# Optimization experiments

Measured on AMD Instinct MI355X. Metric: run time of the kernel, lower is better.

## Reference

```python
import jax, jax.numpy as jnp
import numpy as np

T = 0.2  # temperature (init default)
EPS = 1e-12  # torch F.normalize eps


def setup_inputs() -> dict:
    key = jax.random.key(0)
    k1, k2 = jax.random.split(key, 2)
    b, in_c, out_c = 8192, 128, 128
    anchor_features = jax.random.normal(k1, (b, in_c), dtype=jnp.float32)
    W = jax.random.normal(k2, (in_c, out_c), dtype=jnp.float32) * (1.0 / np.sqrt(in_c))
    bias = jnp.zeros((out_c,), dtype=jnp.float32)
    return {"anchor_features": anchor_features, "W": W, "bias": bias}


def reference(anchor_features, W, bias):
    # MappingLayer: linear projection + L2 normalize, then pairwise cosine sims.
    z = anchor_features @ W + bias                                  # [b, d]
    z = z / jnp.maximum(jnp.linalg.norm(z, axis=-1, keepdims=True), EPS)
    sim = (z @ z.T) / T                                             # [b, b]
    b = sim.shape[0]
    idx = jnp.arange(b)
    j0 = (idx + b // 2) % b                                         # positive pair index
    # Fused symmetric exp matrix: E[i,j] = exp(sim[i,j] + sim[j,i])
    E = jnp.exp(sim + sim.T)                                        # [b, b]
    top = E[idx, j0]                                                # exp(s_ij0 + s_j0i)
    bottom = jnp.sum(E, axis=1) - E[idx, idx]                       # sum over j != i
    loss = -jnp.sum(jnp.log(top / bottom)) / (b - 1)
    return loss
```

## Files before the change

### kernel.cpp

```cpp
#include <hip/hip_runtime.h>
#include <stdint.h>

typedef short bf16x8 __attribute__((ext_vector_type(8)));
typedef float f32x4 __attribute__((ext_vector_type(4)));

#define NROWS 8192
#define DIM   128
#define ZSCALE 3.7982824f
#define LN2F  0.6931471805599453f


__device__ __forceinline__ unsigned short f32_to_bf16_bits(float x) {
  union { float f; uint32_t u; } v; v.f = x;
  uint32_t r = v.u + 0x7FFFu + ((v.u >> 16) & 1u);
  return (unsigned short)(r >> 16);
}

__global__ __launch_bounds__(256) void k_wprep(const float* __restrict__ W,
                                               unsigned short* __restrict__ Wtf,
                                               float* __restrict__ sumexp,
                                               float* __restrict__ topacc) {
  const int idx = blockIdx.x * 256 + threadIdx.x;
  if (idx < 2048) {
    const int l = idx & 63, chunk = idx >> 6;
    const int tj = chunk >> 2, ks = chunk & 3, g = l >> 4, q = l & 15;
    const float* wp = W + (size_t)(ks * 32 + g * 8) * DIM + tj * 16 + q;
    bf16x8 o;
#pragma unroll
    for (int e = 0; e < 8; ++e) o[e] = (short)f32_to_bf16_bits(wp[(size_t)e * DIM]);
    *(bf16x8*)(Wtf + (size_t)idx * 8) = o;
  }
  if (idx < NROWS) sumexp[idx] = 0.f;
  if (idx == 0) topacc[0] = 0.f;
}

__global__ __launch_bounds__(256) void k_proj_norm(
    const float* __restrict__ anchor, const unsigned short* __restrict__ Wtf,
    const float* __restrict__ bias, unsigned short* __restrict__ zf) {
  __shared__ float part[4][16][132];
  const int t = threadIdx.x;
  const int wv = t >> 6, l = t & 63, g = l >> 4, q = l & 15;
  const int rb = blockIdx.x * 16;

  const float* ap = anchor + (size_t)(rb + q) * DIM + wv * 32 + g * 8;
  const f32x4 a0 = *(const f32x4*)ap, a1 = *(const f32x4*)(ap + 4);
  bf16x8 a;
#pragma unroll
  for (int e = 0; e < 4; ++e) {
    a[e] = (short)f32_to_bf16_bits(a0[e]);
    a[4 + e] = (short)f32_to_bf16_bits(a1[e]);
  }

  f32x4 acc[8];
#pragma unroll
  for (int tj = 0; tj < 8; ++tj) acc[tj] = (f32x4){0.f, 0.f, 0.f, 0.f};
#pragma unroll
  for (int tj = 0; tj < 8; ++tj) {
    const bf16x8 b = *(const bf16x8*)(Wtf + (size_t)((tj * 4 + wv) * 64 + l) * 8);
    acc[tj] = __builtin_amdgcn_mfma_f32_16x16x32_bf16(a, b, acc[tj], 0, 0, 0);
  }

#pragma unroll
  for (int tj = 0; tj < 8; ++tj)
#pragma unroll
    for (int r = 0; r < 4; ++r) part[wv][4 * g + r][tj * 16 + q] = acc[tj][r];
  __syncthreads();

  const int row = t >> 4, c = t & 15;
  float v[8];
#pragma unroll
  for (int e = 0; e < 8; ++e) v[e] = bias[c * 8 + e];
#pragma unroll
  for (int s = 0; s < 4; ++s) {
    const f32x4 p0 = *(const f32x4*)&part[s][row][c * 8];
    const f32x4 p1 = *(const f32x4*)&part[s][row][c * 8 + 4];
#pragma unroll
    for (int e = 0; e < 4; ++e) {
      v[e] += p0[e];
      v[4 + e] += p1[e];
    }
  }
  float ss = 0.f;
#pragma unroll
  for (int e = 0; e < 8; ++e) ss += v[e] * v[e];
#pragma unroll
  for (int m = 1; m < 16; m <<= 1) ss += __shfl_xor(ss, m, 64);
  const float inv = ZSCALE / fmaxf(sqrtf(ss), 1e-12f);

  bf16x8 o;
#pragma unroll
  for (int e = 0; e < 8; ++e) o[e] = (short)f32_to_bf16_bits(v[e] * inv);
  const int ks = c >> 2, gg = c & 3;
  *(bf16x8*)(zf + (size_t)(((blockIdx.x * 4 + ks) * 64) + gg * 16 + row) * 8) = o;
}

template <int MODE>
__device__ __forceinline__ void simloss_body(
    const unsigned short* __restrict__ zf, float* __restrict__ sumexp,
    float* __restrict__ topacc, const int r0, const int cb, const int l,
    const int g, const int q) {
  bf16x8 afr[2][4];
#pragma unroll
  for (int ti = 0; ti < 2; ++ti)
#pragma unroll
    for (int ks = 0; ks < 4; ++ks)
      afr[ti][ks] = *(const bf16x8*)(
          zf + (size_t)((((r0 >> 4) + ti) * 4 + ks) * 512 + l * 8));

  float sums[2][4] = {{0.f, 0.f, 0.f, 0.f}, {0.f, 0.f, 0.f, 0.f}};
  float colacc[16];
#pragma unroll
  for (int p = 0; p < 16; ++p) colacc[p] = 0.f;
  float topv = 0.f;
  const int posr = r0 + 4096;

  bool qeq[4];
#pragma unroll
  for (int r = 0; r < 4; ++r) qeq[r] = (q == 4 * g + r);

  auto LOADB = [&](bf16x8 b[4], int c0) {
    const int bcol = c0 >> 4;
#pragma unroll
    for (int ks = 0; ks < 4; ++ks)
      b[ks] = *(const bf16x8*)(zf + (size_t)((bcol * 4 + ks) * 512 + l * 8));
  };
  auto COMPUTE = [&](const bf16x8 b[4], int c0, int step) {
    f32x4 acc[2];
    acc[0] = (f32x4){0.f, 0.f, 0.f, 0.f};
    acc[1] = acc[0];
#pragma unroll
    for (int ti = 0; ti < 2; ++ti)
#pragma unroll
      for (int ks = 0; ks < 4; ++ks)
        acc[ti] = __builtin_amdgcn_mfma_f32_16x16x32_bf16(afr[ti][ks], b[ks],
                                                          acc[ti], 0, 0, 0);
    int dgti = -1, psti = -1;
    if (MODE == 0) {
      const int dgo = c0 - r0;
      dgti = ((unsigned)dgo < 32u) ? (dgo >> 4) : -1;
    }
    if (MODE == 2) {
      const int pso = c0 - posr;
      psti = ((unsigned)pso < 32u) ? (pso >> 4) : -1;
    }
    float cs = 0.f;
#pragma unroll
    for (int ti = 0; ti < 2; ++ti)
#pragma unroll
      for (int r = 0; r < 4; ++r) {
        const float d = acc[ti][r];
        float e = __builtin_amdgcn_exp2f(d);
        if (MODE == 0 && ti == dgti && qeq[r]) e = 0.f;
        if (MODE == 2 && ti == psti && qeq[r]) topv += d;
        sums[ti][r] += e;
        if (MODE != 0) cs += e;
      }
    if (MODE != 0) colacc[step] += cs;
  };

  bf16x8 bA[4], bB[4];
  LOADB(bA, cb);
#pragma unroll
  for (int p = 0; p < 8; ++p) {
    LOADB(bB, cb + p * 32 + 16);
    COMPUTE(bA, cb + p * 32, 2 * p);
    if (p < 7) LOADB(bA, cb + p * 32 + 32);
    COMPUTE(bB, cb + p * 32 + 16, 2 * p + 1);
  }

#pragma unroll
  for (int ti = 0; ti < 2; ++ti)
#pragma unroll
    for (int r = 0; r < 4; ++r) {
#pragma unroll
      for (int m = 1; m < 16; m <<= 1)
        sums[ti][r] += __shfl_xor(sums[ti][r], m, 64);
    }
  if (q == 0) {
#pragma unroll
    for (int ti = 0; ti < 2; ++ti)
#pragma unroll
      for (int r = 0; r < 4; ++r)
        atomicAdd(&sumexp[r0 + ti * 16 + 4 * g + r], sums[ti][r]);
  }

  if (MODE != 0) {
#pragma unroll
    for (int p = 0; p < 16; ++p) {
      colacc[p] += __shfl_xor(colacc[p], 16, 64);
      colacc[p] += __shfl_xor(colacc[p], 32, 64);
    }
    if (l < 16) {
#pragma unroll
      for (int p = 0; p < 16; ++p)
        atomicAdd(&sumexp[cb + p * 16 + q], colacc[p]);
    }
  }

  if (MODE == 2) {
#pragma unroll
    for (int m = 1; m < 64; m <<= 1) topv += __shfl_xor(topv, m, 64);
    if (l == 0) atomicAdd(topacc, 2.f * topv);
  }
}

__global__ __launch_bounds__(512) void k_simloss(
    const unsigned short* __restrict__ zf, float* __restrict__ sumexp,
    float* __restrict__ topacc) {
  const int t = threadIdx.x;
  const int wv = t >> 6, l = t & 63, g = l >> 4, q = l & 15;
  int rem = (int)blockIdx.x, igrp = 0;
  while (rem >= 32 - igrp) { rem -= 32 - igrp; ++igrp; }
  const int jbi = igrp + rem;
  const int r0 = igrp * 256 + wv * 32;
  const int cb = jbi * 256;
  if (igrp == jbi)           simloss_body<0>(zf, sumexp, topacc, r0, cb, l, g, q);
  else if (jbi == igrp + 16) simloss_body<2>(zf, sumexp, topacc, r0, cb, l, g, q);
  else                       simloss_body<1>(zf, sumexp, topacc, r0, cb, l, g, q);
}

__global__ __launch_bounds__(1024) void k_final(const float* __restrict__ sumexp,
                                                const float* __restrict__ topacc,
                                                float* __restrict__ out) {
  __shared__ float red[16];
  const int t = threadIdx.x;
  float s = 0.f;
  for (int r = t; r < NROWS; r += 1024) s += __log2f(sumexp[r]);
#pragma unroll
  for (int m = 1; m < 64; m <<= 1) s += __shfl_xor(s, m, 64);
  if ((t & 63) == 0) red[t >> 6] = s;
  __syncthreads();
  if (t == 0) {
    float S1 = 0.f;
#pragma unroll
    for (int i = 0; i < 16; ++i) S1 += red[i];
    out[0] = LN2F * (S1 - topacc[0]) * (1.0f / (float)(NROWS - 1));
  }
}

extern "C" void kernel_launch(void* const* d_in, const int* in_sizes, int n_in,
                              void* d_out, int out_size, void* d_ws, size_t ws_size,
                              hipStream_t stream) {
  const float* anchor = (const float*)d_in[0];
  const float* W = (const float*)d_in[1];
  const float* bias = (const float*)d_in[2];
  float* out = (float*)d_out;

  char* ws = (char*)d_ws;
  unsigned short* zf = (unsigned short*)ws;
  float* sumexp = (float*)(ws + (size_t)2 * 1024 * 1024);
  float* topacc = (float*)(ws + (size_t)2 * 1024 * 1024 + 32768);
  unsigned short* Wtf = (unsigned short*)(ws + (size_t)2 * 1024 * 1024 + 36864);

  k_wprep<<<dim3(64), dim3(256), 0, stream>>>(W, Wtf, sumexp, topacc);
  k_proj_norm<<<dim3(NROWS / 16), dim3(256), 0, stream>>>(anchor, Wtf, bias, zf);
  k_simloss<<<dim3(528), dim3(512), 0, stream>>>(zf, sumexp, topacc);
  k_final<<<dim3(1), dim3(1024), 0, stream>>>(sumexp, topacc, out);
}
```

Baseline: 43.22 us.

## Use 4 waves of 64 rows each with 4-deep B prefetch ring and LDS column sums

The similarity-loss kernel now runs 256 threads per block, and each wave owns 64 rows (four 16-row tiles) instead of 32. This doubles the reuse of each loaded B fragment across MFMAs and halves the global B loads per tile. B fragments are streamed through a 4-slot register ring that prefetches four column groups ahead. Column partial sums now go to an LDS array via shared atomics, then one global atomic per column after a barrier, replacing the shuffle reductions and per-wave global atomics. The cost is higher register pressure from the 4x4 A fragments plus the ring, which may lower occupancy, and more LDS atomic traffic per step.

```diff
diff --git a/kernel.cpp b/kernel.cpp
--- a/kernel.cpp
+++ b/kernel.cpp
@@ -97,79 +97,78 @@
 template <int MODE>
 __device__ __forceinline__ void simloss_body(
     const unsigned short* __restrict__ zf, float* __restrict__ sumexp,
-    float* __restrict__ topacc, const int r0, const int cb, const int l,
-    const int g, const int q) {
-  bf16x8 afr[2][4];
-#pragma unroll
-  for (int ti = 0; ti < 2; ++ti)
+    float* __restrict__ topacc, float* __restrict__ lds_col, const int r0,
+    const int cb, const int t, const int l, const int g, const int q) {
+  bf16x8 afr[4][4];
+#pragma unroll
+  for (int ti = 0; ti < 4; ++ti)
 #pragma unroll
     for (int ks = 0; ks < 4; ++ks)
       afr[ti][ks] = *(const bf16x8*)(
           zf + (size_t)((((r0 >> 4) + ti) * 4 + ks) * 512 + l * 8));
 
-  float sums[2][4] = {{0.f, 0.f, 0.f, 0.f}, {0.f, 0.f, 0.f, 0.f}};
-  float colacc[16];
-#pragma unroll
-  for (int p = 0; p < 16; ++p) colacc[p] = 0.f;
+  float sums[4][4];
+#pragma unroll
+  for (int ti = 0; ti < 4; ++ti)
+#pragma unroll
+    for (int r = 0; r < 4; ++r) sums[ti][r] = 0.f;
   float topv = 0.f;
   const int posr = r0 + 4096;
 
-  bool qeq[4];
-#pragma unroll
-  for (int r = 0; r < 4; ++r) qeq[r] = (q == 4 * g + r);
-
-  auto LOADB = [&](bf16x8 b[4], int c0) {
-    const int bcol = c0 >> 4;
-#pragma unroll
-    for (int ks = 0; ks < 4; ++ks)
-      b[ks] = *(const bf16x8*)(zf + (size_t)((bcol * 4 + ks) * 512 + l * 8));
-  };
-  auto COMPUTE = [&](const bf16x8 b[4], int c0, int step) {
-    f32x4 acc[2];
-    acc[0] = (f32x4){0.f, 0.f, 0.f, 0.f};
-    acc[1] = acc[0];
-#pragma unroll
-    for (int ti = 0; ti < 2; ++ti)
+  bf16x8 ring[4][4];
+#define LOADG(slot, gi)                                                     \
+  {                                                                         \
+    const int bcol = (cb >> 4) + (gi);                                      \
+    _Pragma("unroll") for (int ks = 0; ks < 4; ++ks) ring[slot][ks] =       \
+        *(const bf16x8*)(zf + (size_t)((bcol * 4 + ks) * 512 + l * 8));     \
+  }
+
+#pragma unroll
+  for (int s = 0; s < 4; ++s) LOADG(s, s);
+
+#pragma unroll
+  for (int k = 0; k < 16; ++k) {
+    const int slot = k & 3;
+    f32x4 acc[4];
+#pragma unroll
+    for (int ti = 0; ti < 4; ++ti) acc[ti] = (f32x4){0.f, 0.f, 0.f, 0.f};
+#pragma unroll
+    for (int ti = 0; ti < 4; ++ti)
 #pragma unroll
       for (int ks = 0; ks < 4; ++ks)
-        acc[ti] = __builtin_amdgcn_mfma_f32_16x16x32_bf16(afr[ti][ks], b[ks],
-                                                          acc[ti], 0, 0, 0);
+        acc[ti] = __builtin_amdgcn_mfma_f32_16x16x32_bf16(
+            afr[ti][ks], ring[slot][ks], acc[ti], 0, 0, 0);
+
+    const int c0 = cb + k * 16;
     int dgti = -1, psti = -1;
     if (MODE == 0) {
       const int dgo = c0 - r0;
-      dgti = ((unsigned)dgo < 32u) ? (dgo >> 4) : -1;
+      dgti = ((unsigned)dgo < 64u) ? (dgo >> 4) : -1;
     }
     if (MODE == 2) {
       const int pso = c0 - posr;
-      psti = ((unsigned)pso < 32u) ? (pso >> 4) : -1;
+      psti = ((unsigned)pso < 64u) ? (pso >> 4) : -1;
     }
     float cs = 0.f;
 #pragma unroll
-    for (int ti = 0; ti < 2; ++ti)
+    for (int ti = 0; ti < 4; ++ti)
 #pragma unroll
       for (int r = 0; r < 4; ++r) {
         const float d = acc[ti][r];
         float e = __builtin_amdgcn_exp2f(d);
-        if (MODE == 0 && ti == dgti && qeq[r]) e = 0.f;
-        if (MODE == 2 && ti == psti && qeq[r]) topv += d;
+        if (MODE == 0 && ti == dgti && q == 4 * g + r) e = 0.f;
+        if (MODE == 2 && ti == psti && q == 4 * g + r) topv += d;
         sums[ti][r] += e;
         if (MODE != 0) cs += e;
       }
-    if (MODE != 0) colacc[step] += cs;
-  };
-
-  bf16x8 bA[4], bB[4];
-  LOADB(bA, cb);
-#pragma unroll
-  for (int p = 0; p < 8; ++p) {
-    LOADB(bB, cb + p * 32 + 16);
-    COMPUTE(bA, cb + p * 32, 2 * p);
-    if (p < 7) LOADB(bA, cb + p * 32 + 32);
-    COMPUTE(bB, cb + p * 32 + 16, 2 * p + 1);
-  }
-
-#pragma unroll
-  for (int ti = 0; ti < 2; ++ti)
+    if (MODE != 0) atomicAdd(&lds_col[k * 16 + q], cs);
+
+    if (k + 4 < 16) LOADG(slot, k + 4);
+  }
+#undef LOADG
+
+#pragma unroll
+  for (int ti = 0; ti < 4; ++ti)
 #pragma unroll
     for (int r = 0; r < 4; ++r) {
 #pragma unroll
@@ -178,23 +177,15 @@
     }
   if (q == 0) {
 #pragma unroll
-    for (int ti = 0; ti < 2; ++ti)
+    for (int ti = 0; ti < 4; ++ti)
 #pragma unroll
       for (int r = 0; r < 4; ++r)
         atomicAdd(&sumexp[r0 + ti * 16 + 4 * g + r], sums[ti][r]);
   }
 
   if (MODE != 0) {
-#pragma unroll
-    for (int p = 0; p < 16; ++p) {
-      colacc[p] += __shfl_xor(colacc[p], 16, 64);
-      colacc[p] += __shfl_xor(colacc[p], 32, 64);
-    }
-    if (l < 16) {
-#pragma unroll
-      for (int p = 0; p < 16; ++p)
-        atomicAdd(&sumexp[cb + p * 16 + q], colacc[p]);
-    }
+    __syncthreads();
+    atomicAdd(&sumexp[cb + t], lds_col[t]);
   }
 
   if (MODE == 2) {
@@ -204,19 +195,26 @@
   }
 }
 
-__global__ __launch_bounds__(512) void k_simloss(
+__global__ __launch_bounds__(256) void k_simloss(
     const unsigned short* __restrict__ zf, float* __restrict__ sumexp,
     float* __restrict__ topacc) {
+  __shared__ float lds_col[256];
   const int t = threadIdx.x;
   const int wv = t >> 6, l = t & 63, g = l >> 4, q = l & 15;
+  lds_col[t] = 0.f;
+  __syncthreads();
+
   int rem = (int)blockIdx.x, igrp = 0;
   while (rem >= 32 - igrp) { rem -= 32 - igrp; ++igrp; }
   const int jbi = igrp + rem;
-  const int r0 = igrp * 256 + wv * 32;
+  const int r0 = igrp * 256 + wv * 64;
   const int cb = jbi * 256;
-  if (igrp == jbi)           simloss_body<0>(zf, sumexp, topacc, r0, cb, l, g, q);
-  else if (jbi == igrp + 16) simloss_body<2>(zf, sumexp, topacc, r0, cb, l, g, q);
-  else                       simloss_body<1>(zf, sumexp, topacc, r0, cb, l, g, q);
+  if (igrp == jbi)
+    simloss_body<0>(zf, sumexp, topacc, lds_col, r0, cb, t, l, g, q);
+  else if (jbi == igrp + 16)
+    simloss_body<2>(zf, sumexp, topacc, lds_col, r0, cb, t, l, g, q);
+  else
+    simloss_body<1>(zf, sumexp, topacc, lds_col, r0, cb, t, l, g, q);
 }
 
 __global__ __launch_bounds__(1024) void k_final(const float* __restrict__ sumexp,
@@ -254,6 +252,6 @@
 
   k_wprep<<<dim3(64), dim3(256), 0, stream>>>(W, Wtf, sumexp, topacc);
   k_proj_norm<<<dim3(NROWS / 16), dim3(256), 0, stream>>>(anchor, Wtf, bias, zf);
-  k_simloss<<<dim3(528), dim3(512), 0, stream>>>(zf, sumexp, topacc);
+  k_simloss<<<dim3(528), dim3(256), 0, stream>>>(zf, sumexp, topacc);
   k_final<<<dim3(1), dim3(1024), 0, stream>>>(sumexp, topacc, out);
 }
```

Measured after the change: 46.30 us. 1.07x slower.
